# Optimization experiments

Hardware: AMD Instinct MI355X
Metric: run time of the kernel (lower is better)

## Reference

```python
import jax, jax.numpy as jnp
import numpy as np

N_S = 50000
N_T = 50000
E = 800000
D_IN = 128
D_OUT = 128


def setup_inputs() -> dict:
    key = jax.random.key(0)
    k1, k2, k3, k4 = jax.random.split(key, 4)
    edge_index = jax.random.randint(k1, (2, E), 0, N_S, dtype=jnp.int64)
    x_s = jax.random.normal(k2, (N_S, D_IN), dtype=jnp.float32)
    x_t = jax.random.normal(k3, (N_T, D_IN), dtype=jnp.float32)
    # glorot-ish linear weight of GCNConv (bias=False)
    W = jax.random.normal(k4, (D_IN, D_OUT), dtype=jnp.float32) * (1.0 / np.sqrt(D_IN))
    return {"edge_index": edge_index, "x_s": x_s, "x_t": x_t, "W": W}


def reference(edge_index, x_s, x_t, W):
    N_s = x_s.shape[0]
    N_t = x_t.shape[0]
    N = N_s + N_t
    # dropout p=0.0 -> identity; concat bipartite features
    x = jnp.concatenate([x_s, x_t], axis=0)  # [N, d_in]
    row = edge_index[0]
    col = edge_index[1] + N_s  # module shifts target indices in-place
    # GCNConv: add self-loops with weight 1
    loops = jnp.arange(N, dtype=row.dtype)
    row_f = jnp.concatenate([row, loops])
    col_f = jnp.concatenate([col, loops])
    w = jnp.ones(row_f.shape[0], dtype=x.dtype)
    # symmetric degree normalization: deg computed on target (col)
    deg = jax.ops.segment_sum(w, col_f, num_segments=N)
    deg_inv_sqrt = jnp.where(deg > 0, jax.lax.rsqrt(deg), 0.0)
    norm = deg_inv_sqrt[row_f] * deg_inv_sqrt[col_f]  # [E+N]
    # linear transform then normalized scatter-add aggregation
    h = x @ W  # [N, d_out]
    msg = h[row_f] * norm[:, None]  # gather + scale, [E+N, d_out]
    out = jax.ops.segment_sum(msg, col_f, num_segments=N)  # scatter-add
    out = jax.nn.relu(out)
    return out[:N_s], out[N_s:]
```

## Files before the change

### kernel.cpp

```cpp
#include <hip/hip_runtime.h>
#include <math.h>

#define NSRC 50000
#define NTGT 50000
#define NTOT 100000
#define NEDGE 800000
#define DIM 128
#define WPAD 136
#define CHUNKS_PER_BLK 2
#define GEMM_GRID 782

#define NBUCK 196
#define PBLK 98
#define EPB 8192
#define SCAN_N (NBUCK * PBLK)
#define SCAN_PER_THR 19
#define BCAP 6144

typedef __attribute__((ext_vector_type(8))) short short8;
typedef __attribute__((ext_vector_type(4))) float float4v;

__device__ __forceinline__ unsigned short f2bf(float f) {
    unsigned u = __float_as_uint(f);
    unsigned r = (u + 0x7FFFu + ((u >> 16) & 1u)) >> 16;
    return (unsigned short)r;
}
__device__ __forceinline__ float bf2f(unsigned us) {
    return __uint_as_float(us << 16);
}

__global__ void k_prep(const float* __restrict__ W, unsigned short* __restrict__ Wt) {
    int i = blockIdx.x * blockDim.x + threadIdx.x;
    if (i < DIM * DIM) {
        int k = i >> 7, n = i & 127;
        Wt[n * DIM + k] = f2bf(W[i]);
    }
}

__global__ __launch_bounds__(1024) void k_count(const int* __restrict__ col,
                                                int* __restrict__ H) {
    __shared__ int hist[NBUCK];
    int tid = threadIdx.x;
    if (tid < NBUCK) hist[tid] = 0;
    __syncthreads();
    int e0 = blockIdx.x * EPB;
    for (int i = tid; i < EPB; i += 1024) {
        int e = e0 + i;
        if (e < NEDGE) atomicAdd(&hist[col[e] >> 8], 1);
    }
    __syncthreads();
    if (tid < NBUCK) H[tid * PBLK + blockIdx.x] = hist[tid];
}

__global__ __launch_bounds__(1024) void k_scan(int* __restrict__ H) {
    __shared__ int P[1024], Q[1024];
    int tid = threadIdx.x;
    int base = tid * SCAN_PER_THR;
    int v[SCAN_PER_THR];
    int s = 0;
#pragma unroll
    for (int i = 0; i < SCAN_PER_THR; ++i) {
        int idx = base + i;
        int x = (idx < SCAN_N) ? H[idx] : 0;
        v[i] = s;
        s += x;
    }
    P[tid] = s;
    int* src = P; int* dst = Q;
    for (int d = 1; d < 1024; d <<= 1) {
        __syncthreads();
        dst[tid] = src[tid] + ((tid >= d) ? src[tid - d] : 0);
        int* t = src; src = dst; dst = t;
    }
    __syncthreads();
    int excl = src[tid] - s;
#pragma unroll
    for (int i = 0; i < SCAN_PER_THR; ++i) {
        int idx = base + i;
        if (idx < SCAN_N) H[idx] = excl + v[i];
    }
}

__global__ __launch_bounds__(1024) void k_part(const int* __restrict__ row,
                                               const int* __restrict__ col,
                                               const int* __restrict__ S,
                                               unsigned* __restrict__ part) {
    __shared__ int cur[NBUCK];
    int tid = threadIdx.x;
    if (tid < NBUCK) cur[tid] = S[tid * PBLK + blockIdx.x];
    __syncthreads();
    int e0 = blockIdx.x * EPB;
    for (int i = tid; i < EPB; i += 1024) {
        int e = e0 + i;
        if (e < NEDGE) {
            int c = col[e];
            int q = c >> 8;
            int pos = atomicAdd(&cur[q], 1);
            part[pos] = (unsigned)row[e] | ((unsigned)(c & 255) << 16);
        }
    }
}

__global__ __launch_bounds__(1024) void k_bucket(const int* __restrict__ S,
                                                 const unsigned* __restrict__ part,
                                                 int* __restrict__ csr,
                                                 int* __restrict__ tstart,
                                                 int* __restrict__ tcnt) {
    __shared__ unsigned ebuf[BCAP];
    __shared__ unsigned short srt[BCAP];
    __shared__ int hist[256], bufA[256], bufB[256], cur[256];

    int q = blockIdx.x, tid = threadIdx.x;
    int base = S[q * PBLK];
    int end = (q == NBUCK - 1) ? NEDGE : S[(q + 1) * PBLK];
    int n = end - base;

    if (tid < 256) hist[tid] = 0;
    __syncthreads();
    for (int i = tid; i < n; i += 1024) {
        unsigned p = part[base + i];
        ebuf[i] = p;
        atomicAdd(&hist[p >> 16], 1);
    }
    __syncthreads();

    if (tid < 256) bufA[tid] = hist[tid];
    int* src = bufA; int* dst = bufB;
    for (int d = 1; d < 256; d <<= 1) {
        __syncthreads();
        if (tid < 256) dst[tid] = src[tid] + ((tid >= d) ? src[tid - d] : 0);
        int* t = src; src = dst; dst = t;
    }
    __syncthreads();
    if (tid < 256) {
        int excl = src[tid] - hist[tid];
        cur[tid] = excl;
        int c = q * 256 + tid;
        if (c < NTGT) {
            tstart[c] = base + excl;
            tcnt[c] = hist[tid];
        }
    }
    __syncthreads();

    for (int i = tid; i < n; i += 1024) {
        unsigned p = ebuf[i];
        int pos = atomicAdd(&cur[p >> 16], 1);
        srt[pos] = (unsigned short)(p & 0xffffu);
    }
    __syncthreads();
    for (int i = tid; i < n; i += 1024) csr[base + i] = (int)srt[i];
}

__global__ __launch_bounds__(256) void k_gemm(const float* __restrict__ xsrc,
                                              const float* __restrict__ xtgt,
                                              const unsigned short* __restrict__ Wt,
                                              unsigned short* __restrict__ h,
                                              float* __restrict__ out) {
    __shared__ unsigned short Bs[128 * WPAD];
    __shared__ unsigned short Hs[64 * 128];

    const int tid = threadIdx.x;

    for (int idx = tid; idx < 2048; idx += 256) {
        int n = idx >> 4, c8 = idx & 15;
        uint4 v = *(const uint4*)(Wt + n * DIM + c8 * 8);
        *(uint4*)&Bs[n * WPAD + c8 * 8] = v;
    }
    __syncthreads();

    const int wave = tid >> 6, lane = tid & 63;
    const int nl = lane & 15, quad = lane >> 4;

    for (int ch = 0; ch < CHUNKS_PER_BLK; ++ch) {
        const int base = (blockIdx.x * CHUNKS_PER_BLK + ch) * 64;
        if (base >= NTOT) break;

        int m = base + wave * 16 + nl;
        int mc = (m < NTOT) ? m : (NTOT - 1);
        const float* xrow = (mc < NSRC) ? (xsrc + (size_t)mc * DIM)
                                        : (xtgt + (size_t)(mc - NSRC) * DIM);

        float4v acc[8];
#pragma unroll
        for (int t = 0; t < 8; ++t) acc[t] = (float4v){0.f, 0.f, 0.f, 0.f};

#pragma unroll
        for (int s = 0; s < 4; ++s) {
            int k0 = s * 32 + quad * 8;
            float4 a0 = *(const float4*)(xrow + k0);
            float4 a1 = *(const float4*)(xrow + k0 + 4);
            short8 af;
            af[0] = (short)f2bf(a0.x); af[1] = (short)f2bf(a0.y);
            af[2] = (short)f2bf(a0.z); af[3] = (short)f2bf(a0.w);
            af[4] = (short)f2bf(a1.x); af[5] = (short)f2bf(a1.y);
            af[6] = (short)f2bf(a1.z); af[7] = (short)f2bf(a1.w);
#pragma unroll
            for (int t = 0; t < 8; ++t) {
                short8 bf = *(const short8*)&Bs[(t * 16 + nl) * WPAD + k0];
                acc[t] = __builtin_amdgcn_mfma_f32_16x16x32_bf16(af, bf, acc[t], 0, 0, 0);
            }
        }

        if (ch) __syncthreads();
#pragma unroll
        for (int t = 0; t < 8; ++t)
#pragma unroll
            for (int r = 0; r < 4; ++r)
                Hs[(wave * 16 + quad * 4 + r) * 128 + t * 16 + nl] = f2bf(acc[t][r]);
        __syncthreads();

#pragma unroll
        for (int j = 0; j < 4; ++j) {
            int off_us = tid * 8 + j * 2048;
            int g = base + (off_us >> 7);
            int colc = off_us & 127;
            if (g < NTOT) {
                uint4 v = *(const uint4*)&Hs[off_us];
                *(uint4*)(h + (size_t)g * DIM + colc) = v;
                if (g < NSRC) {
                    unsigned pk[4] = {v.x, v.y, v.z, v.w};
                    float4 o0, o1;
                    o0.x = fmaxf(bf2f(pk[0] & 0xffff), 0.f);
                    o0.y = fmaxf(bf2f(pk[0] >> 16), 0.f);
                    o0.z = fmaxf(bf2f(pk[1] & 0xffff), 0.f);
                    o0.w = fmaxf(bf2f(pk[1] >> 16), 0.f);
                    o1.x = fmaxf(bf2f(pk[2] & 0xffff), 0.f);
                    o1.y = fmaxf(bf2f(pk[2] >> 16), 0.f);
                    o1.z = fmaxf(bf2f(pk[3] & 0xffff), 0.f);
                    o1.w = fmaxf(bf2f(pk[3] >> 16), 0.f);
                    float* op = out + (size_t)g * DIM + colc;
                    *(float4*)op = o0;
                    *(float4*)(op + 4) = o1;
                }
            }
        }
    }
}

__global__ __launch_bounds__(256) void k_agg(const int* __restrict__ tstart,
                                             const int* __restrict__ tcnt,
                                             const int* __restrict__ csr,
                                             const unsigned short* __restrict__ h,
                                             float* __restrict__ out) {
    int w = threadIdx.x >> 6;
    int lane = threadIdx.x & 63;
    int c = blockIdx.x * 4 + w;
    if (c >= NTGT) return;

    int n = tcnt[c];
    int s0 = tstart[c];
    int half = lane >> 5;
    int hl = lane & 31;

    float4 sum = make_float4(0.f, 0.f, 0.f, 0.f);
    int j = 0;
    while (j < n) {
        int nb = (n - j < 64) ? (n - j) : 64;
        int v = (lane < nb) ? csr[s0 + j + lane] : 0;
        int npair = nb & ~1;
        int kk = 0;
#pragma unroll 8
        for (; kk < npair; kk += 2) {
            int r = __shfl(v, kk + half, 64);
            uint2 d = *(const uint2*)(h + (size_t)r * DIM + hl * 4);
            sum.x += bf2f(d.x & 0xffff); sum.y += bf2f(d.x >> 16);
            sum.z += bf2f(d.y & 0xffff); sum.w += bf2f(d.y >> 16);
        }
        if (kk < nb) {
            int r = __shfl(v, kk, 64);
            if (half == 0) {
                uint2 d = *(const uint2*)(h + (size_t)r * DIM + hl * 4);
                sum.x += bf2f(d.x & 0xffff); sum.y += bf2f(d.x >> 16);
                sum.z += bf2f(d.y & 0xffff); sum.w += bf2f(d.y >> 16);
            }
        }
        j += nb;
    }

    float4 tot;
    tot.x = sum.x + __shfl(sum.x, lane ^ 32, 64);
    tot.y = sum.y + __shfl(sum.y, lane ^ 32, 64);
    tot.z = sum.z + __shfl(sum.z, lane ^ 32, 64);
    tot.w = sum.w + __shfl(sum.w, lane ^ 32, 64);

    if (half == 0) {
        float di = rsqrtf(1.0f + (float)n);
        float dd = di * di;
        uint2 dh = *(const uint2*)(h + (size_t)(NSRC + c) * DIM + hl * 4);
        float4 o;
        o.x = fmaxf(di * tot.x + dd * bf2f(dh.x & 0xffff), 0.f);
        o.y = fmaxf(di * tot.y + dd * bf2f(dh.x >> 16), 0.f);
        o.z = fmaxf(di * tot.z + dd * bf2f(dh.y & 0xffff), 0.f);
        o.w = fmaxf(di * tot.w + dd * bf2f(dh.y >> 16), 0.f);
        *(float4*)(out + (size_t)(NSRC + c) * DIM + hl * 4) = o;
    }
}

extern "C" void kernel_launch(void* const* d_in, const int* in_sizes, int n_in,
                              void* d_out, int out_size, void* d_ws, size_t ws_size,
                              hipStream_t stream) {
    const int* ei     = (const int*)d_in[0];
    const float* xsrc = (const float*)d_in[1];
    const float* xtgt = (const float*)d_in[2];
    const float* W    = (const float*)d_in[3];
    float* out = (float*)d_out;

    const int* row = ei;
    const int* col = ei + NEDGE;

    char* ws = (char*)d_ws;
    unsigned short* h  = (unsigned short*)ws;  ws += (size_t)NTOT * DIM * 2;
    unsigned short* Wt = (unsigned short*)ws;  ws += DIM * DIM * 2;
    unsigned* part = (unsigned*)ws;            ws += (size_t)NEDGE * 4;
    int* csr    = (int*)ws;                    ws += (size_t)NEDGE * 4;
    int* S      = (int*)ws;                    ws += 19456 * 4;
    int* tstart = (int*)ws;                    ws += NTGT * 4;
    int* tcnt   = (int*)ws;                    ws += NTGT * 4;

    k_prep<<<(DIM * DIM + 255) / 256, 256, 0, stream>>>(W, Wt);
    k_count<<<PBLK, 1024, 0, stream>>>(col, S);
    k_scan<<<1, 1024, 0, stream>>>(S);
    k_part<<<PBLK, 1024, 0, stream>>>(row, col, S, part);
    k_bucket<<<NBUCK, 1024, 0, stream>>>(S, part, csr, tstart, tcnt);
    k_gemm<<<GEMM_GRID, 256, 0, stream>>>(xsrc, xtgt, Wt, h, out);
    k_agg<<<(NTGT + 3) / 4, 256, 0, stream>>>(tstart, tcnt, csr, h, out);
}
```

Measured before the change: 196.2 us.

## Replace count/scan/partition with atomic fixed-capacity buckets, 16-bit CSR, wider gather

```diff
diff --git a/kernel.cpp b/kernel.cpp
--- a/kernel.cpp
+++ b/kernel.cpp
@@ -13,8 +13,6 @@
 #define NBUCK 196
 #define PBLK 98
 #define EPB 8192
-#define SCAN_N (NBUCK * PBLK)
-#define SCAN_PER_THR 19
 #define BCAP 6144
 
 typedef __attribute__((ext_vector_type(8))) short short8;
@@ -29,81 +27,45 @@
     return __uint_as_float(us << 16);
 }
 
-__global__ void k_prep(const float* __restrict__ W, unsigned short* __restrict__ Wt) {
+__global__ void k_prep(const float* __restrict__ W, unsigned short* __restrict__ Wt,
+                       int* __restrict__ bcnt) {
     int i = blockIdx.x * blockDim.x + threadIdx.x;
+    if (i < NBUCK) bcnt[i] = 0;
     if (i < DIM * DIM) {
         int k = i >> 7, n = i & 127;
         Wt[n * DIM + k] = f2bf(W[i]);
     }
 }
 
-__global__ __launch_bounds__(1024) void k_count(const int* __restrict__ col,
-                                                int* __restrict__ H) {
-    __shared__ int hist[NBUCK];
+__global__ __launch_bounds__(1024) void k_part2(const int* __restrict__ row,
+                                                const int* __restrict__ col,
+                                                int* __restrict__ bcnt,
+                                                unsigned* __restrict__ part) {
+    __shared__ int hist[NBUCK], runbase[NBUCK], cur[NBUCK];
     int tid = threadIdx.x;
     if (tid < NBUCK) hist[tid] = 0;
     __syncthreads();
     int e0 = blockIdx.x * EPB;
-    for (int i = tid; i < EPB; i += 1024) {
-        int e = e0 + i;
-        if (e < NEDGE) atomicAdd(&hist[col[e] >> 8], 1);
-    }
-    __syncthreads();
-    if (tid < NBUCK) H[tid * PBLK + blockIdx.x] = hist[tid];
-}
-
-__global__ __launch_bounds__(1024) void k_scan(int* __restrict__ H) {
-    __shared__ int P[1024], Q[1024];
-    int tid = threadIdx.x;
-    int base = tid * SCAN_PER_THR;
-    int v[SCAN_PER_THR];
-    int s = 0;
-#pragma unroll
-    for (int i = 0; i < SCAN_PER_THR; ++i) {
-        int idx = base + i;
-        int x = (idx < SCAN_N) ? H[idx] : 0;
-        v[i] = s;
-        s += x;
-    }
-    P[tid] = s;
-    int* src = P; int* dst = Q;
-    for (int d = 1; d < 1024; d <<= 1) {
-        __syncthreads();
-        dst[tid] = src[tid] + ((tid >= d) ? src[tid - d] : 0);
-        int* t = src; src = dst; dst = t;
-    }
-    __syncthreads();
-    int excl = src[tid] - s;
-#pragma unroll
-    for (int i = 0; i < SCAN_PER_THR; ++i) {
-        int idx = base + i;
-        if (idx < SCAN_N) H[idx] = excl + v[i];
-    }
-}
-
-__global__ __launch_bounds__(1024) void k_part(const int* __restrict__ row,
-                                               const int* __restrict__ col,
-                                               const int* __restrict__ S,
-                                               unsigned* __restrict__ part) {
-    __shared__ int cur[NBUCK];
-    int tid = threadIdx.x;
-    if (tid < NBUCK) cur[tid] = S[tid * PBLK + blockIdx.x];
-    __syncthreads();
-    int e0 = blockIdx.x * EPB;
-    for (int i = tid; i < EPB; i += 1024) {
-        int e = e0 + i;
-        if (e < NEDGE) {
-            int c = col[e];
-            int q = c >> 8;
-            int pos = atomicAdd(&cur[q], 1);
-            part[pos] = (unsigned)row[e] | ((unsigned)(c & 255) << 16);
-        }
-    }
-}
-
-__global__ __launch_bounds__(1024) void k_bucket(const int* __restrict__ S,
+    int eend = (e0 + EPB < NEDGE) ? e0 + EPB : NEDGE;
+    for (int e = e0 + tid; e < eend; e += 1024)
+        atomicAdd(&hist[col[e] >> 8], 1);
+    __syncthreads();
+    if (tid < NBUCK) {
+        runbase[tid] = atomicAdd(&bcnt[tid], hist[tid]);
+        cur[tid] = 0;
+    }
+    __syncthreads();
+    for (int e = e0 + tid; e < eend; e += 1024) {
+        int c = col[e];
+        int q = c >> 8;
+        int pos = runbase[q] + atomicAdd(&cur[q], 1);
+        part[q * BCAP + pos] = (unsigned)row[e] | ((unsigned)(c & 255) << 16);
+    }
+}
+
+__global__ __launch_bounds__(1024) void k_bucket(const int* __restrict__ bcnt,
                                                  const unsigned* __restrict__ part,
-                                                 int* __restrict__ csr,
+                                                 unsigned short* __restrict__ csr,
                                                  int* __restrict__ tstart,
                                                  int* __restrict__ tcnt) {
     __shared__ unsigned ebuf[BCAP];
@@ -111,9 +73,8 @@
     __shared__ int hist[256], bufA[256], bufB[256], cur[256];
 
     int q = blockIdx.x, tid = threadIdx.x;
-    int base = S[q * PBLK];
-    int end = (q == NBUCK - 1) ? NEDGE : S[(q + 1) * PBLK];
-    int n = end - base;
+    int n = bcnt[q];
+    int base = q * BCAP;
 
     if (tid < 256) hist[tid] = 0;
     __syncthreads();
@@ -149,7 +110,9 @@
         srt[pos] = (unsigned short)(p & 0xffffu);
     }
     __syncthreads();
-    for (int i = tid; i < n; i += 1024) csr[base + i] = (int)srt[i];
+    int m = (n + 1) >> 1;
+    unsigned* dst32 = (unsigned*)(csr + base);
+    for (int i = tid; i < m; i += 1024) dst32[i] = ((unsigned*)srt)[i];
 }
 
 __global__ __launch_bounds__(256) void k_gemm(const float* __restrict__ xsrc,
@@ -240,7 +203,7 @@
 
 __global__ __launch_bounds__(256) void k_agg(const int* __restrict__ tstart,
                                              const int* __restrict__ tcnt,
-                                             const int* __restrict__ csr,
+                                             const unsigned short* __restrict__ csr,
                                              const unsigned short* __restrict__ h,
                                              float* __restrict__ out) {
     int w = threadIdx.x >> 6;
@@ -250,50 +213,65 @@
 
     int n = tcnt[c];
     int s0 = tstart[c];
-    int half = lane >> 5;
-    int hl = lane & 31;
-
-    float4 sum = make_float4(0.f, 0.f, 0.f, 0.f);
+    int q = lane >> 4;
+    int ql = lane & 15;
+
+    float acc[8];
+#pragma unroll
+    for (int i = 0; i < 8; ++i) acc[i] = 0.f;
+
     int j = 0;
     while (j < n) {
         int nb = (n - j < 64) ? (n - j) : 64;
-        int v = (lane < nb) ? csr[s0 + j + lane] : 0;
-        int npair = nb & ~1;
+        int v = (lane < nb) ? (int)csr[s0 + j + lane] : 0;
+        int n4 = nb & ~3;
         int kk = 0;
-#pragma unroll 8
-        for (; kk < npair; kk += 2) {
-            int r = __shfl(v, kk + half, 64);
-            uint2 d = *(const uint2*)(h + (size_t)r * DIM + hl * 4);
-            sum.x += bf2f(d.x & 0xffff); sum.y += bf2f(d.x >> 16);
-            sum.z += bf2f(d.y & 0xffff); sum.w += bf2f(d.y >> 16);
-        }
-        if (kk < nb) {
-            int r = __shfl(v, kk, 64);
-            if (half == 0) {
-                uint2 d = *(const uint2*)(h + (size_t)r * DIM + hl * 4);
-                sum.x += bf2f(d.x & 0xffff); sum.y += bf2f(d.x >> 16);
-                sum.z += bf2f(d.y & 0xffff); sum.w += bf2f(d.y >> 16);
+#pragma unroll 4
+        for (; kk < n4; kk += 4) {
+            int r = __shfl(v, kk + q, 64);
+            uint4 d = *(const uint4*)(h + (size_t)r * DIM + ql * 8);
+            acc[0] += bf2f(d.x & 0xffff); acc[1] += bf2f(d.x >> 16);
+            acc[2] += bf2f(d.y & 0xffff); acc[3] += bf2f(d.y >> 16);
+            acc[4] += bf2f(d.z & 0xffff); acc[5] += bf2f(d.z >> 16);
+            acc[6] += bf2f(d.w & 0xffff); acc[7] += bf2f(d.w >> 16);
+        }
+        int rem = nb - kk;
+        if (rem) {
+            int qq = (q < rem) ? q : 0;
+            int r = __shfl(v, kk + qq, 64);
+            if (q < rem) {
+                uint4 d = *(const uint4*)(h + (size_t)r * DIM + ql * 8);
+                acc[0] += bf2f(d.x & 0xffff); acc[1] += bf2f(d.x >> 16);
+                acc[2] += bf2f(d.y & 0xffff); acc[3] += bf2f(d.y >> 16);
+                acc[4] += bf2f(d.z & 0xffff); acc[5] += bf2f(d.z >> 16);
+                acc[6] += bf2f(d.w & 0xffff); acc[7] += bf2f(d.w >> 16);
             }
         }
         j += nb;
     }
 
-    float4 tot;
-    tot.x = sum.x + __shfl(sum.x, lane ^ 32, 64);
-    tot.y = sum.y + __shfl(sum.y, lane ^ 32, 64);
-    tot.z = sum.z + __shfl(sum.z, lane ^ 32, 64);
-    tot.w = sum.w + __shfl(sum.w, lane ^ 32, 64);
-
-    if (half == 0) {
+#pragma unroll
+    for (int i = 0; i < 8; ++i) {
+        acc[i] += __shfl_xor(acc[i], 16, 64);
+        acc[i] += __shfl_xor(acc[i], 32, 64);
+    }
+
+    if (q == 0) {
         float di = rsqrtf(1.0f + (float)n);
         float dd = di * di;
-        uint2 dh = *(const uint2*)(h + (size_t)(NSRC + c) * DIM + hl * 4);
-        float4 o;
-        o.x = fmaxf(di * tot.x + dd * bf2f(dh.x & 0xffff), 0.f);
-        o.y = fmaxf(di * tot.y + dd * bf2f(dh.x >> 16), 0.f);
-        o.z = fmaxf(di * tot.z + dd * bf2f(dh.y & 0xffff), 0.f);
-        o.w = fmaxf(di * tot.w + dd * bf2f(dh.y >> 16), 0.f);
-        *(float4*)(out + (size_t)(NSRC + c) * DIM + hl * 4) = o;
+        uint4 dh = *(const uint4*)(h + (size_t)(NSRC + c) * DIM + ql * 8);
+        float4 o0, o1;
+        o0.x = fmaxf(di * acc[0] + dd * bf2f(dh.x & 0xffff), 0.f);
+        o0.y = fmaxf(di * acc[1] + dd * bf2f(dh.x >> 16), 0.f);
+        o0.z = fmaxf(di * acc[2] + dd * bf2f(dh.y & 0xffff), 0.f);
+        o0.w = fmaxf(di * acc[3] + dd * bf2f(dh.y >> 16), 0.f);
+        o1.x = fmaxf(di * acc[4] + dd * bf2f(dh.z & 0xffff), 0.f);
+        o1.y = fmaxf(di * acc[5] + dd * bf2f(dh.z >> 16), 0.f);
+        o1.z = fmaxf(di * acc[6] + dd * bf2f(dh.w & 0xffff), 0.f);
+        o1.w = fmaxf(di * acc[7] + dd * bf2f(dh.w >> 16), 0.f);
+        float* op = out + (size_t)(NSRC + c) * DIM + ql * 8;
+        *(float4*)op = o0;
+        *(float4*)(op + 4) = o1;
     }
 }
 
@@ -312,17 +290,15 @@
     char* ws = (char*)d_ws;
     unsigned short* h  = (unsigned short*)ws;  ws += (size_t)NTOT * DIM * 2;
     unsigned short* Wt = (unsigned short*)ws;  ws += DIM * DIM * 2;
-    unsigned* part = (unsigned*)ws;            ws += (size_t)NEDGE * 4;
-    int* csr    = (int*)ws;                    ws += (size_t)NEDGE * 4;
-    int* S      = (int*)ws;                    ws += 19456 * 4;
+    unsigned* part = (unsigned*)ws;            ws += (size_t)NBUCK * BCAP * 4;
+    unsigned short* csr = (unsigned short*)ws; ws += (size_t)NBUCK * BCAP * 2;
+    int* bcnt   = (int*)ws;                    ws += NBUCK * 4;
     int* tstart = (int*)ws;                    ws += NTGT * 4;
     int* tcnt   = (int*)ws;                    ws += NTGT * 4;
 
-    k_prep<<<(DIM * DIM + 255) / 256, 256, 0, stream>>>(W, Wt);
-    k_count<<<PBLK, 1024, 0, stream>>>(col, S);
-    k_scan<<<1, 1024, 0, stream>>>(S);
-    k_part<<<PBLK, 1024, 0, stream>>>(row, col, S, part);
-    k_bucket<<<NBUCK, 1024, 0, stream>>>(S, part, csr, tstart, tcnt);
+    k_prep<<<(DIM * DIM + 255) / 256, 256, 0, stream>>>(W, Wt, bcnt);
+    k_part2<<<PBLK, 1024, 0, stream>>>(row, col, bcnt, part);
+    k_bucket<<<NBUCK, 1024, 0, stream>>>(bcnt, part, csr, tstart, tcnt);
     k_gemm<<<GEMM_GRID, 256, 0, stream>>>(xsrc, xtgt, Wt, h, out);
     k_agg<<<(NTGT + 3) / 4, 256, 0, stream>>>(tstart, tcnt, csr, h, out);
 }
```

Result: faster. 171.3 us (-12.7%).
